# Kernel optimization log

Hardware: AMD Instinct MI355X
Metric: run time of the kernel (lower is better)

## Reference

```python
import jax, jax.numpy as jnp
import numpy as np

# Module constants from CheckboxDetector.__init__ / _postprocess
N = 8192            # candidate detections
C = 2               # checkbox classes (checked / unchecked)
THR = 0.7           # confidence threshold (self.threshold)
IOU_THR = 0.5       # torchvision.ops.nms iou_threshold
INPUT_H, INPUT_W = 1280.0, 1280.0   # self.input_shape
IMG_H, IMG_W = 2480.0, 3508.0       # original image (A4 @ 300dpi)
SCALER = max(IMG_W / INPUT_W, IMG_H / INPUT_H)
EPS = 1e-9


def setup_inputs() -> dict:
    key = jax.random.key(0)
    k1, k2, k3 = jax.random.split(key, 3)
    cls_conf = jax.random.uniform(k1, (N, C), dtype=jnp.float32)
    # well-formed xyxy boxes inside the 1280x1280 canvas
    xy = jax.random.uniform(k2, (N, 2), dtype=jnp.float32, minval=0.0, maxval=1200.0)
    wh = jax.random.uniform(k3, (N, 2), dtype=jnp.float32, minval=8.0, maxval=80.0)
    bboxes = jnp.concatenate([xy, xy + wh], axis=1)  # [N,4]
    return {"cls_conf": cls_conf, "bboxes": bboxes}


def _pairwise_iou(boxes):
    # boxes: [N,4] xyxy -> iou: [N,N]
    x1, y1, x2, y2 = boxes[:, 0], boxes[:, 1], boxes[:, 2], boxes[:, 3]
    area = (x2 - x1) * (y2 - y1)
    iw = jnp.clip(jnp.minimum(x2[:, None], x2[None, :]) - jnp.maximum(x1[:, None], x1[None, :]), 0.0)
    ih = jnp.clip(jnp.minimum(y2[:, None], y2[None, :]) - jnp.maximum(y1[:, None], y1[None, :]), 0.0)
    inter = iw * ih
    return inter / (area[:, None] + area[None, :] - inter + EPS)


def reference(cls_conf, bboxes):
    # _threshold: keep rows with any class confidence > THR (mask instead of
    # dynamic filtering, for fixed shapes under jit)
    valid = jnp.any(cls_conf > THR, axis=1)            # [N]
    scores = jnp.max(cls_conf, axis=1)                 # cls_conf.max(1)
    masked_scores = jnp.where(valid, scores, -jnp.inf)

    # _nms: sort by score desc, greedy IoU suppression (torchvision semantics)
    order = jnp.argsort(-masked_scores)
    b = bboxes[order]          # [N,4]
    c = cls_conf[order]        # [N,C]
    v = valid[order]           # [N]

    iou = _pairwise_iou(b)     # [N,N]  (256 MB: memory-bound core)
    idx = jnp.arange(N)

    def body(i, keep):
        # box i (if still kept & valid) suppresses later boxes overlapping > IOU_THR
        sup = (iou[i] > IOU_THR) & (idx > i) & keep[i]
        return keep & ~sup

    keep = jax.lax.fori_loop(0, N, body, v)            # [N] bool

    # _postprocess tail: rescale boxes to original image size; suppressed
    # detections are zeroed (mask semantics in place of dynamic gather).
    kf = keep.astype(cls_conf.dtype)[:, None]
    boxes_out = b * SCALER * kf                        # [N,4]
    conf_out = c * kf                                  # [N,C]
    return jnp.concatenate([boxes_out, conf_out], axis=1)  # [N, 4+C]
```

## Files before the change

### kernel.cpp

```cpp
#include <hip/hip_runtime.h>
#include <math.h>

#define N_BOX 8192
#define NW 128
#define NTHR 512
#define LCAP 24576
#define NRBLK 256
#define NPTILE 576
#define WPB 8
#define NWAVE (NPTILE * WPB)
#define SLOT 128
#define WSPT (NWAVE / NTHR)
#define NCH 16
#define THR_C 0.7f
#define IOU_THR_C 0.5f
#define EPS_C 1e-9f

__device__ __constant__ float kScaler = (float)(3508.0 / 1280.0);

static __device__ __forceinline__ unsigned long long key_from(float c0, float c1, int i) {
    bool valid = (c0 > THR_C) || (c1 > THR_C);
    float ms = valid ? fmaxf(c0, c1) : -INFINITY;
    unsigned int u = __float_as_uint(ms);
    unsigned int m = (u & 0x80000000u) ? ~u : (u | 0x80000000u);
    unsigned int d = ~m;
    return ((unsigned long long)d << 32) | (unsigned int)i;
}

__global__ __launch_bounds__(NTHR) void stageA(const float* __restrict__ conf,
                                               const float* __restrict__ bboxes,
                                               int* __restrict__ partial,
                                               unsigned int* __restrict__ wcnt,
                                               unsigned int* __restrict__ wslot) {
    int b = blockIdx.x;
    int t = threadIdx.x;
    if (b < NRBLK) {
        __shared__ unsigned long long ck[512];
        int ech = b >> 4;
        int cch = b & 15;
        {
            int j = (cch << 9) + t;
            float2 cc = ((const float2*)conf)[j];
            ck[t] = key_from(cc.x, cc.y, j);
        }
        __syncthreads();
        int i = (ech << 9) + t;
        float2 ci = ((const float2*)conf)[i];
        unsigned long long ki = key_from(ci.x, ci.y, i);
        const ulonglong2* ckp = (const ulonglong2*)ck;
        int a0 = 0, a1 = 0, a2 = 0, a3 = 0;
#pragma unroll 4
        for (int l = 0; l < 256; l += 2) {
            ulonglong2 u = ckp[l];
            ulonglong2 v = ckp[l + 1];
            a0 += (u.x < ki) ? 1 : 0;
            a1 += (u.y < ki) ? 1 : 0;
            a2 += (v.x < ki) ? 1 : 0;
            a3 += (v.y < ki) ? 1 : 0;
        }
        partial[cch * N_BOX + i] = (a0 + a1) + (a2 + a3);
    } else {
        int pb = b - NRBLK;
        int g = 0;
        while (8 * (g + 1) * (g + 2) <= pb) ++g;
        int off = pb - 8 * g * (g + 1);
        int wq = off / (g + 1);
        int w = (g << 4) + wq;
        int h = off - wq * (g + 1);
        int waveid = pb * WPB + (t >> 6);
        int lane = t & 63;
        __shared__ float4 cb[64];
        __shared__ float ca02[64];
        __shared__ unsigned long long cbk[64];
        __shared__ unsigned char cjr[64];
        __shared__ unsigned long long jvS;
        __shared__ int nvjS;
        if (t < 64) {
            int j = (w << 6) + t;
            float2 cc = ((const float2*)conf)[j];
            bool v = (cc.x > THR_C) || (cc.y > THR_C);
            unsigned long long bv = __ballot(v);
            if (v) {
                int pos = __popcll(bv & ((1ull << t) - 1ull));
                float4 c = ((const float4*)bboxes)[j];
                cb[pos] = c;
                ca02[pos] = 0.2f * ((c.z - c.x) * (c.w - c.y));
                cbk[pos] = key_from(cc.x, cc.y, j);
                cjr[pos] = (unsigned char)t;
            }
            if (t == 0) { jvS = bv; nvjS = __popcll(bv); }
        }
        __syncthreads();
        unsigned long long jv = jvS;
        int nvj = nvjS;
        int ibase = h << 10;
        float4 rb0, rb1;
        float raF0, raF1, raS0, raS1;
        unsigned long long ki0, ki1;
        int km0, km1;
        {
            int i = ibase + t;
            int rel = i - (w << 6);
            float2 cc = ((const float2*)conf)[i];
            bool iv = (cc.x > THR_C) || (cc.y > THR_C);
            if (!iv || rel >= 63)      km0 = 64;
            else if (rel >= 0)         km0 = __popcll(jv & ((2ull << rel) - 1ull));
            else                       km0 = 0;
            rb0 = ((const float4*)bboxes)[i];
            raF0 = (rb0.z - rb0.x) * (rb0.w - rb0.y);
            raS0 = 0.2f * raF0;
            ki0 = key_from(cc.x, cc.y, i);
        }
        {
            int i = ibase + 512 + t;
            int rel = i - (w << 6);
            float2 cc = ((const float2*)conf)[i];
            bool iv = (cc.x > THR_C) || (cc.y > THR_C);
            if (!iv || rel >= 63)      km1 = 64;
            else if (rel >= 0)         km1 = __popcll(jv & ((2ull << rel) - 1ull));
            else                       km1 = 0;
            rb1 = ((const float4*)bboxes)[i];
            raF1 = (rb1.z - rb1.x) * (rb1.w - rb1.y);
            raS1 = 0.2f * raF1;
            ki1 = key_from(cc.x, cc.y, i);
        }
        int wc = 0;
        if (__any((km0 < nvj) || (km1 < nvj))) {
            unsigned long long bits0 = 0ull, bits1 = 0ull;
            for (int bb = 0; bb < nvj; ++bb) {
                float4 c = cb[bb];
                float s2 = ca02[bb];
                float iw0 = fminf(rb0.z, c.z) - fmaxf(rb0.x, c.x);
                float ih0 = fminf(rb0.w, c.w) - fmaxf(rb0.y, c.y);
                float inter0 = fmaxf(iw0, 0.0f) * fmaxf(ih0, 0.0f);
                if (inter0 > raS0 + s2) {
                    float caF = (c.z - c.x) * (c.w - c.y);
                    float iou = inter0 / (raF0 + caF - inter0 + EPS_C);
                    if (iou > IOU_THR_C) bits0 |= (1ull << bb);
                }
                float iw1 = fminf(rb1.z, c.z) - fmaxf(rb1.x, c.x);
                float ih1 = fminf(rb1.w, c.w) - fmaxf(rb1.y, c.y);
                float inter1 = fmaxf(iw1, 0.0f) * fmaxf(ih1, 0.0f);
                if (inter1 > raS1 + s2) {
                    float caF = (c.z - c.x) * (c.w - c.y);
                    float iou = inter1 / (raF1 + caF - inter1 + EPS_C);
                    if (iou > IOU_THR_C) bits1 |= (1ull << bb);
                }
            }
            {
                unsigned long long m = (km0 >= 64) ? 0ull : (~0ull << km0);
                unsigned long long eb = bits0 & m;
                if (__any(eb != 0ull)) {
                    int ec = __popcll(eb);
                    int pre = ec;
#pragma unroll
                    for (int d = 1; d < 64; d <<= 1) {
                        int vv = __shfl_up(pre, d, 64);
                        if (lane >= d) pre += vv;
                    }
                    int tot = __shfl(pre, 63, 64);
                    int idx = wc + pre - ec;
                    unsigned long long tb = eb;
                    int i = ibase + t;
                    while (tb) {
                        int bb = __builtin_ctzll(tb); tb &= tb - 1;
                        if (idx < SLOT) {
                            int j = (w << 6) + (int)cjr[bb];
                            unsigned int e = (ki0 < cbk[bb])
                                             ? (((unsigned int)i << 13) | (unsigned int)j)
                                             : (((unsigned int)j << 13) | (unsigned int)i);
                            wslot[(size_t)waveid * SLOT + idx] = e;
                        }
                        ++idx;
                    }
                    wc += tot;
                }
            }
            {
                unsigned long long m = (km1 >= 64) ? 0ull : (~0ull << km1);
                unsigned long long eb = bits1 & m;
                if (__any(eb != 0ull)) {
                    int ec = __popcll(eb);
                    int pre = ec;
#pragma unroll
                    for (int d = 1; d < 64; d <<= 1) {
                        int vv = __shfl_up(pre, d, 64);
                        if (lane >= d) pre += vv;
                    }
                    int tot = __shfl(pre, 63, 64);
                    int idx = wc + pre - ec;
                    unsigned long long tb = eb;
                    int i = ibase + 512 + t;
                    while (tb) {
                        int bb = __builtin_ctzll(tb); tb &= tb - 1;
                        if (idx < SLOT) {
                            int j = (w << 6) + (int)cjr[bb];
                            unsigned int e = (ki1 < cbk[bb])
                                             ? (((unsigned int)i << 13) | (unsigned int)j)
                                             : (((unsigned int)j << 13) | (unsigned int)i);
                            wslot[(size_t)waveid * SLOT + idx] = e;
                        }
                        ++idx;
                    }
                    wc += tot;
                }
            }
        }
        if (lane == 0) wcnt[waveid] = (unsigned int)wc;
    }
}

__global__ __launch_bounds__(NTHR) void stageB(const float* __restrict__ conf,
                                               const float* __restrict__ bboxes,
                                               const int* __restrict__ partial,
                                               const unsigned int* __restrict__ wcnt,
                                               const unsigned int* __restrict__ wslot,
                                               float* __restrict__ out) {
    __shared__ unsigned int eL[LCAP];
    __shared__ unsigned long long kL[NW], tL[NW], vL[NW];
    __shared__ int wsum[NTHR];
    __shared__ int chg[3];
    __shared__ int fbF, nvF;
    int t = threadIdx.x;
    if (t == 0) { fbF = 0; nvF = 0; chg[0] = 0; chg[1] = 0; chg[2] = 0; }
    for (int base = 0; base < N_BOX; base += NTHR) {
        int i = base + t;
        float2 cc = ((const float2*)conf)[i];
        unsigned long long bv = __ballot((cc.x > THR_C) || (cc.y > THR_C));
        if ((t & 63) == 0) vL[i >> 6] = bv;
    }
    int nq[WSPT], myo[WSPT];
    int s = 0;
    bool ov = false;
#pragma unroll
    for (int q = 0; q < WSPT; ++q) {
        int v = (int)wcnt[t * WSPT + q];
        nq[q] = v; myo[q] = s; s += v;
        if (v > SLOT) ov = true;
    }
    wsum[t] = s;
    __syncthreads();
    if (t < NW) kL[t] = vL[t];
    for (int off = 1; off < NTHR; off <<= 1) {
        int v = (t >= off) ? wsum[t - off] : 0;
        __syncthreads();
        wsum[t] += v;
        __syncthreads();
    }
    int ebase = wsum[t] - s;
    int totE = wsum[NTHR - 1];
    if (ov || totE > LCAP) fbF = 1;
    __syncthreads();
    int fb = fbF;
    if (!fb) {
#pragma unroll
        for (int q = 0; q < WSPT; ++q) {
            int w2 = t * WSPT + q;
            int off = ebase + myo[q];
            for (int k = 0; k < nq[q]; ++k)
                eL[off + k] = wslot[(size_t)w2 * SLOT + k];
        }
    }
    __syncthreads();
    if (!fb) {
        for (int it = 0; it < N_BOX; ++it) {
            if (t < NW) tL[t] = 0ull;
            __syncthreads();
            for (int e = t; e < totE; e += NTHR) {
                unsigned int ed = eL[e];
                int src = (int)(ed >> 13);
                if ((kL[src >> 6] >> (src & 63)) & 1ull) {
                    int tg = (int)(ed & 8191u);
                    atomicOr(&tL[tg >> 6], 1ull << (tg & 63));
                }
            }
            __syncthreads();
            if (t < NW) {
                unsigned long long nk = vL[t] & ~tL[t];
                if (nk != kL[t]) chg[it % 3] = 1;
                kL[t] = nk;
            }
            if (t == 0) chg[(it + 2) % 3] = 0;
            __syncthreads();
            if (chg[it % 3] == 0) break;
        }
    } else {
        unsigned int* sinv = eL;
        for (int base = 0; base < N_BOX; base += NTHR) {
            int i = base + t;
            int r = 0;
#pragma unroll
            for (int c = 0; c < NCH; ++c) r += partial[c * N_BOX + i];
            sinv[r] = (unsigned int)i;
        }
        if (t < NW) { atomicAdd(&nvF, __popcll(vL[t])); tL[t] = 0ull; kL[t] = 0ull; }
        __syncthreads();
        int nv = nvF;
        if (t < 64) {
            for (int a = 0; a < nv - 1; ++a) {
                bool rem = (tL[a >> 6] >> (a & 63)) & 1ull;
                if (!rem) {
                    float4 r = ((const float4*)bboxes)[sinv[a]];
                    float ra = (r.z - r.x) * (r.w - r.y);
                    for (int b2 = a + 1 + t; b2 < nv; b2 += 64) {
                        float4 c = ((const float4*)bboxes)[sinv[b2]];
                        float ca = (c.z - c.x) * (c.w - c.y);
                        float iw = fminf(r.z, c.z) - fmaxf(r.x, c.x);
                        float ih = fminf(r.w, c.w) - fmaxf(r.y, c.y);
                        iw = fmaxf(iw, 0.0f);
                        ih = fmaxf(ih, 0.0f);
                        float inter = iw * ih;
                        float iou = inter / (ra + ca - inter + EPS_C);
                        if (iou > IOU_THR_C) atomicOr(&tL[b2 >> 6], 1ull << (b2 & 63));
                    }
                }
            }
        }
        __syncthreads();
        for (int a = t; a < nv; a += NTHR) {
            if (!((tL[a >> 6] >> (a & 63)) & 1ull)) {
                int ia = (int)sinv[a];
                atomicOr(&kL[ia >> 6], 1ull << (ia & 63));
            }
        }
    }
    __syncthreads();
    for (int base = 0; base < N_BOX; base += NTHR) {
        int i = base + t;
        int r = 0;
#pragma unroll
        for (int c = 0; c < NCH; ++c) r += partial[c * N_BOX + i];
        bool kept = (kL[i >> 6] >> (i & 63)) & 1ull;
        if (kept) {
            float4 bx = ((const float4*)bboxes)[i];
            float2 cc = ((const float2*)conf)[i];
            out[r * 6 + 0] = bx.x * kScaler;
            out[r * 6 + 1] = bx.y * kScaler;
            out[r * 6 + 2] = bx.z * kScaler;
            out[r * 6 + 3] = bx.w * kScaler;
            out[r * 6 + 4] = cc.x;
            out[r * 6 + 5] = cc.y;
        } else {
            out[r * 6 + 0] = 0.0f;
            out[r * 6 + 1] = 0.0f;
            out[r * 6 + 2] = 0.0f;
            out[r * 6 + 3] = 0.0f;
            out[r * 6 + 4] = 0.0f;
            out[r * 6 + 5] = 0.0f;
        }
    }
}

extern "C" void kernel_launch(void* const* d_in, const int* in_sizes, int n_in,
                              void* d_out, int out_size, void* d_ws, size_t ws_size,
                              hipStream_t stream) {
    const float* cls_conf = (const float*)d_in[0];
    const float* bboxes   = (const float*)d_in[1];
    float* out = (float*)d_out;

    char* ws = (char*)d_ws;
    int*          partial = (int*)(ws + 0);
    unsigned int* wcnt    = (unsigned int*)(ws + 524288);
    unsigned int* wslot   = (unsigned int*)(ws + 557056);
    (void)ws_size; (void)in_sizes; (void)n_in; (void)out_size;

    stageA<<<NRBLK + NPTILE, NTHR, 0, stream>>>(cls_conf, bboxes, partial, wcnt, wslot);
    stageB<<<1, NTHR, 0, stream>>>(cls_conf, bboxes, partial, wcnt, wslot, out);
}
```

Baseline: 102.6 us.

## Trim single-block stage: precompute valid mask, wave-level scan, interleaved rank partials

The rank-count stage now uses 8 chunks of 1024 keys instead of 16 of 512. Its partial counts are stored interleaved per box, so the single-block final stage can read them with two int4 loads. Stage A also writes the validity ballot words, which removes a full pass over the confidences in stage B. Stage B's block-wide scan with many __syncthreads is replaced by a wave shuffle scan plus a tiny cross-wave step. Box loads in the pair tiles are deferred until a tile actually has work. The cost is fewer and longer rank blocks in stage A.

```diff
diff --git a/kernel.cpp b/kernel.cpp
--- a/kernel.cpp
+++ b/kernel.cpp
@@ -5,13 +5,13 @@
 #define NW 128
 #define NTHR 512
 #define LCAP 24576
-#define NRBLK 256
+#define NRBLK 128
 #define NPTILE 576
 #define WPB 8
 #define NWAVE (NPTILE * WPB)
 #define SLOT 128
 #define WSPT (NWAVE / NTHR)
-#define NCH 16
+#define NCH 8
 #define THR_C 0.7f
 #define IOU_THR_C 0.5f
 #define EPS_C 1e-9f
@@ -30,27 +30,33 @@
 __global__ __launch_bounds__(NTHR) void stageA(const float* __restrict__ conf,
                                                const float* __restrict__ bboxes,
                                                int* __restrict__ partial,
+                                               unsigned long long* __restrict__ validw,
                                                unsigned int* __restrict__ wcnt,
                                                unsigned int* __restrict__ wslot) {
     int b = blockIdx.x;
     int t = threadIdx.x;
     if (b < NRBLK) {
-        __shared__ unsigned long long ck[512];
-        int ech = b >> 4;
-        int cch = b & 15;
-        {
-            int j = (cch << 9) + t;
+        __shared__ unsigned long long ck[1024];
+        int ech = b >> 3;
+        int cch = b & 7;
+        for (int l = t; l < 1024; l += NTHR) {
+            int j = (cch << 10) + l;
             float2 cc = ((const float2*)conf)[j];
-            ck[t] = key_from(cc.x, cc.y, j);
+            ck[l] = key_from(cc.x, cc.y, j);
         }
         __syncthreads();
         int i = (ech << 9) + t;
         float2 ci = ((const float2*)conf)[i];
+        bool iv = (ci.x > THR_C) || (ci.y > THR_C);
+        if (cch == 0) {
+            unsigned long long bv = __ballot(iv);
+            if ((t & 63) == 0) validw[i >> 6] = bv;
+        }
         unsigned long long ki = key_from(ci.x, ci.y, i);
         const ulonglong2* ckp = (const ulonglong2*)ck;
         int a0 = 0, a1 = 0, a2 = 0, a3 = 0;
 #pragma unroll 4
-        for (int l = 0; l < 256; l += 2) {
+        for (int l = 0; l < 512; l += 2) {
             ulonglong2 u = ckp[l];
             ulonglong2 v = ckp[l + 1];
             a0 += (u.x < ki) ? 1 : 0;
@@ -58,7 +64,7 @@
             a2 += (v.x < ki) ? 1 : 0;
             a3 += (v.y < ki) ? 1 : 0;
         }
-        partial[cch * N_BOX + i] = (a0 + a1) + (a2 + a3);
+        partial[i * NCH + cch] = (a0 + a1) + (a2 + a3);
     } else {
         int pb = b - NRBLK;
         int g = 0;
@@ -94,38 +100,35 @@
         unsigned long long jv = jvS;
         int nvj = nvjS;
         int ibase = h << 10;
-        float4 rb0, rb1;
-        float raF0, raF1, raS0, raS1;
-        unsigned long long ki0, ki1;
+        int i0 = ibase + t;
+        int i1 = i0 + 512;
+        float2 cc0 = ((const float2*)conf)[i0];
+        float2 cc1 = ((const float2*)conf)[i1];
         int km0, km1;
         {
-            int i = ibase + t;
-            int rel = i - (w << 6);
-            float2 cc = ((const float2*)conf)[i];
-            bool iv = (cc.x > THR_C) || (cc.y > THR_C);
+            int rel = i0 - (w << 6);
+            bool iv = (cc0.x > THR_C) || (cc0.y > THR_C);
             if (!iv || rel >= 63)      km0 = 64;
             else if (rel >= 0)         km0 = __popcll(jv & ((2ull << rel) - 1ull));
             else                       km0 = 0;
-            rb0 = ((const float4*)bboxes)[i];
-            raF0 = (rb0.z - rb0.x) * (rb0.w - rb0.y);
-            raS0 = 0.2f * raF0;
-            ki0 = key_from(cc.x, cc.y, i);
         }
         {
-            int i = ibase + 512 + t;
-            int rel = i - (w << 6);
-            float2 cc = ((const float2*)conf)[i];
-            bool iv = (cc.x > THR_C) || (cc.y > THR_C);
+            int rel = i1 - (w << 6);
+            bool iv = (cc1.x > THR_C) || (cc1.y > THR_C);
             if (!iv || rel >= 63)      km1 = 64;
             else if (rel >= 0)         km1 = __popcll(jv & ((2ull << rel) - 1ull));
             else                       km1 = 0;
-            rb1 = ((const float4*)bboxes)[i];
-            raF1 = (rb1.z - rb1.x) * (rb1.w - rb1.y);
-            raS1 = 0.2f * raF1;
-            ki1 = key_from(cc.x, cc.y, i);
         }
         int wc = 0;
         if (__any((km0 < nvj) || (km1 < nvj))) {
+            float4 rb0 = ((const float4*)bboxes)[i0];
+            float4 rb1 = ((const float4*)bboxes)[i1];
+            float raF0 = (rb0.z - rb0.x) * (rb0.w - rb0.y);
+            float raF1 = (rb1.z - rb1.x) * (rb1.w - rb1.y);
+            float raS0 = 0.2f * raF0;
+            float raS1 = 0.2f * raF1;
+            unsigned long long ki0 = key_from(cc0.x, cc0.y, i0);
+            unsigned long long ki1 = key_from(cc1.x, cc1.y, i1);
             unsigned long long bits0 = 0ull, bits1 = 0ull;
             for (int bb = 0; bb < nvj; ++bb) {
                 float4 c = cb[bb];
@@ -161,14 +164,13 @@
                     int tot = __shfl(pre, 63, 64);
                     int idx = wc + pre - ec;
                     unsigned long long tb = eb;
-                    int i = ibase + t;
                     while (tb) {
                         int bb = __builtin_ctzll(tb); tb &= tb - 1;
                         if (idx < SLOT) {
                             int j = (w << 6) + (int)cjr[bb];
                             unsigned int e = (ki0 < cbk[bb])
-                                             ? (((unsigned int)i << 13) | (unsigned int)j)
-                                             : (((unsigned int)j << 13) | (unsigned int)i);
+                                             ? (((unsigned int)i0 << 13) | (unsigned int)j)
+                                             : (((unsigned int)j << 13) | (unsigned int)i0);
                             wslot[(size_t)waveid * SLOT + idx] = e;
                         }
                         ++idx;
@@ -190,14 +192,13 @@
                     int tot = __shfl(pre, 63, 64);
                     int idx = wc + pre - ec;
                     unsigned long long tb = eb;
-                    int i = ibase + 512 + t;
                     while (tb) {
                         int bb = __builtin_ctzll(tb); tb &= tb - 1;
                         if (idx < SLOT) {
                             int j = (w << 6) + (int)cjr[bb];
                             unsigned int e = (ki1 < cbk[bb])
-                                             ? (((unsigned int)i << 13) | (unsigned int)j)
-                                             : (((unsigned int)j << 13) | (unsigned int)i);
+                                             ? (((unsigned int)i1 << 13) | (unsigned int)j)
+                                             : (((unsigned int)j << 13) | (unsigned int)i1);
                             wslot[(size_t)waveid * SLOT + idx] = e;
                         }
                         ++idx;
@@ -213,22 +214,21 @@
 __global__ __launch_bounds__(NTHR) void stageB(const float* __restrict__ conf,
                                                const float* __restrict__ bboxes,
                                                const int* __restrict__ partial,
+                                               const unsigned long long* __restrict__ validw,
                                                const unsigned int* __restrict__ wcnt,
                                                const unsigned int* __restrict__ wslot,
                                                float* __restrict__ out) {
     __shared__ unsigned int eL[LCAP];
     __shared__ unsigned long long kL[NW], tL[NW], vL[NW];
-    __shared__ int wsum[NTHR];
+    __shared__ int wsum[WPB];
+    __shared__ int totS;
     __shared__ int chg[3];
     __shared__ int fbF, nvF;
     int t = threadIdx.x;
+    int lane = t & 63;
+    int wv = t >> 6;
     if (t == 0) { fbF = 0; nvF = 0; chg[0] = 0; chg[1] = 0; chg[2] = 0; }
-    for (int base = 0; base < N_BOX; base += NTHR) {
-        int i = base + t;
-        float2 cc = ((const float2*)conf)[i];
-        unsigned long long bv = __ballot((cc.x > THR_C) || (cc.y > THR_C));
-        if ((t & 63) == 0) vL[i >> 6] = bv;
-    }
+    if (t < NW) { unsigned long long v = validw[t]; vL[t] = v; kL[t] = v; }
     int nq[WSPT], myo[WSPT];
     int s = 0;
     bool ov = false;
@@ -238,17 +238,23 @@
         nq[q] = v; myo[q] = s; s += v;
         if (v > SLOT) ov = true;
     }
-    wsum[t] = s;
-    __syncthreads();
-    if (t < NW) kL[t] = vL[t];
-    for (int off = 1; off < NTHR; off <<= 1) {
-        int v = (t >= off) ? wsum[t - off] : 0;
-        __syncthreads();
-        wsum[t] += v;
-        __syncthreads();
-    }
-    int ebase = wsum[t] - s;
-    int totE = wsum[NTHR - 1];
+    int pre = s;
+#pragma unroll
+    for (int d = 1; d < 64; d <<= 1) {
+        int v = __shfl_up(pre, d, 64);
+        if (lane >= d) pre += v;
+    }
+    if (lane == 63) wsum[wv] = pre;
+    __syncthreads();
+    if (t == 0) {
+        int acc = 0;
+#pragma unroll
+        for (int q = 0; q < WPB; ++q) { int v = wsum[q]; wsum[q] = acc; acc += v; }
+        totS = acc;
+    }
+    __syncthreads();
+    int ebase = wsum[wv] + (pre - s);
+    int totE = totS;
     if (ov || totE > LCAP) fbF = 1;
     __syncthreads();
     int fb = fbF;
@@ -290,7 +296,7 @@
             int i = base + t;
             int r = 0;
 #pragma unroll
-            for (int c = 0; c < NCH; ++c) r += partial[c * N_BOX + i];
+            for (int c = 0; c < NCH; ++c) r += partial[i * NCH + c];
             sinv[r] = (unsigned int)i;
         }
         if (t < NW) { atomicAdd(&nvF, __popcll(vL[t])); tL[t] = 0ull; kL[t] = 0ull; }
@@ -325,11 +331,12 @@
         }
     }
     __syncthreads();
+    const int4* p4 = (const int4*)partial;
     for (int base = 0; base < N_BOX; base += NTHR) {
         int i = base + t;
-        int r = 0;
-#pragma unroll
-        for (int c = 0; c < NCH; ++c) r += partial[c * N_BOX + i];
+        int4 pa = p4[i * 2];
+        int4 pb2 = p4[i * 2 + 1];
+        int r = ((pa.x + pa.y) + (pa.z + pa.w)) + ((pb2.x + pb2.y) + (pb2.z + pb2.w));
         bool kept = (kL[i >> 6] >> (i & 63)) & 1ull;
         if (kept) {
             float4 bx = ((const float4*)bboxes)[i];
@@ -359,11 +366,12 @@
     float* out = (float*)d_out;
 
     char* ws = (char*)d_ws;
-    int*          partial = (int*)(ws + 0);
-    unsigned int* wcnt    = (unsigned int*)(ws + 524288);
-    unsigned int* wslot   = (unsigned int*)(ws + 557056);
+    int*                partial = (int*)(ws + 0);
+    unsigned int*       wcnt    = (unsigned int*)(ws + 262144);
+    unsigned long long* validw  = (unsigned long long*)(ws + 282624);
+    unsigned int*       wslot   = (unsigned int*)(ws + 286720);
     (void)ws_size; (void)in_sizes; (void)n_in; (void)out_size;
 
-    stageA<<<NRBLK + NPTILE, NTHR, 0, stream>>>(cls_conf, bboxes, partial, wcnt, wslot);
-    stageB<<<1, NTHR, 0, stream>>>(cls_conf, bboxes, partial, wcnt, wslot, out);
+    stageA<<<NRBLK + NPTILE, NTHR, 0, stream>>>(cls_conf, bboxes, partial, validw, wcnt, wslot);
+    stageB<<<1, NTHR, 0, stream>>>(cls_conf, bboxes, partial, validw, wcnt, wslot, out);
 }
```

New measurement: 100.1 us. -2.5%, faster.
